# Kernel optimization log

Hardware: AMD Instinct MI355X
Metric: run time of the kernel (lower is better)

The kernel has to match this reference:

```python
import jax, jax.numpy as jnp
import numpy as np

N = 50000      # nodes
E = 800000     # edges
D_IN = 128     # embedding_in
EP = 200000    # prediction edge pairs
CONV_DIMS = [D_IN, 128, 64, 32]
LIN_DIMS = [32, 16, 8, 1]


def setup_inputs() -> dict:
    key = jax.random.key(0)
    ks = jax.random.split(key, 20)
    inp = {
        "x": jax.random.normal(ks[0], (N, D_IN), dtype=jnp.float32),
        "edge_index": jax.random.randint(ks[1], (2, E), 0, N, dtype=jnp.int64 if jax.config.jax_enable_x64 else jnp.int32),
        "pred_edges": jax.random.randint(ks[2], (EP, 2), 0, N, dtype=jnp.int64 if jax.config.jax_enable_x64 else jnp.int32),
    }
    k = 3
    for i in range(3):  # GCNConv weights [in,out] + bias (torch GCNConv has bias)
        din, dout = CONV_DIMS[i], CONV_DIMS[i + 1]
        inp[f"cw{i}"] = jax.random.normal(ks[k], (din, dout), dtype=jnp.float32) / np.sqrt(din); k += 1
        inp[f"cb{i}"] = jax.random.normal(ks[k], (dout,), dtype=jnp.float32) * 0.01; k += 1
    for i in range(3):  # Linear weights stored [in,out]
        din, dout = LIN_DIMS[i], LIN_DIMS[i + 1]
        inp[f"lw{i}"] = jax.random.normal(ks[k], (din, dout), dtype=jnp.float32) / np.sqrt(din); k += 1
        inp[f"lb{i}"] = jax.random.normal(ks[k], (dout,), dtype=jnp.float32) * 0.01; k += 1
    return inp


def gcn_conv(x, W, b, src, dst, n):
    """PyG GCNConv: D^-1/2 (A + I) D^-1/2 X W + b, deg over dst incl. self-loop."""
    h = x @ W  # [n, dout]
    deg = jax.ops.segment_sum(jnp.ones_like(dst, dtype=h.dtype), dst, num_segments=n) + 1.0
    dis = jax.lax.rsqrt(deg)  # deg >= 1 (self loop)
    msg = h[src] * (dis[src] * dis[dst])[:, None]      # gather + per-edge normalize
    out = jax.ops.segment_sum(msg, dst, num_segments=n)  # scatter-add into targets
    out = out + h * (dis * dis)[:, None]                # self-loop contribution
    return out + b


def reference(x, edge_index, pred_edges, cw0, cb0, cw1, cb1, cw2, cb2,
              lw0, lb0, lw1, lb1, lw2, lb2):
    src, dst = edge_index[0], edge_index[1]
    n = x.shape[0]
    for W, b in ((cw0, cb0), (cw1, cb1), (cw2, cb2)):
        x = jax.nn.relu(gcn_conv(x, W, b, src, dst, n))
    x = jax.nn.relu(x @ lw0 + lb0)
    x = jax.nn.relu(x @ lw1 + lb1)
    x = jax.nn.sigmoid(x @ lw2 + lb2)  # [n, 1]
    s = x[:, 0]
    # x[pred_edges] -> [EP,2,1]; mul of pair, transpose+flatten -> [EP]
    return s[pred_edges[:, 0]] * s[pred_edges[:, 1]]
```

## Files before the change

kernel.cpp:

```cpp
#include <hip/hip_runtime.h>
#include <math.h>

constexpr int NN  = 50000;
constexpr int NP  = 50048;
constexpr int NE  = 800000;
constexpr int NEP = 200000;

constexpr int NBKT  = 256;
constexpr int CAP   = 4096;
constexpr int CAPC  = 4096;
constexpr int CHUNK = 4096;

constexpr int BKB = (NE + CHUNK - 1) / CHUNK;
constexpr int W0B = 128 * 128 / 256;
constexpr int W1B = 128 * 64 / 256;
constexpr int W2B = 64 * 32 / 256;
constexpr int FRONT_BLOCKS = BKB + W0B + W1B + W2B;

constexpr int NODE_BLKS32 = (NN + 31) / 32;

typedef _Float16 half8_t __attribute__((ext_vector_type(8)));
typedef float    float4_t __attribute__((ext_vector_type(4)));

static inline int cdiv(long long a, int b) { return (int)((a + b - 1) / b); }

__global__ __launch_bounds__(256) void k_front(const int* __restrict__ src,
        const int* __restrict__ dst, int* __restrict__ binCnt,
        unsigned int* __restrict__ ebuf,
        const float* __restrict__ cw0, _Float16* __restrict__ WT0,
        const float* __restrict__ cw1, _Float16* __restrict__ WT1,
        const float* __restrict__ cw2, _Float16* __restrict__ WT2) {
    const int tid = threadIdx.x;
    const int bid = blockIdx.x;

    if (bid < BKB) {
        __shared__ int hist[NBKT];
        __shared__ int base[NBKT];
        __shared__ int cur[NBKT];
        constexpr int J = CHUNK / 256;
        const int e0 = bid * CHUNK;
        hist[tid] = 0;
        __syncthreads();
        int  s[J], bn[J], dl[J];
        bool ok[J];
#pragma unroll
        for (int j = 0; j < J; ++j) {
            int i = e0 + j * 256 + tid;
            ok[j] = i < NE;
            if (ok[j]) {
                int d = dst[i];
                s[j]  = src[i];
                bn[j] = d >> 8;
                dl[j] = d & 255;
                atomicAdd(&hist[bn[j]], 1);
            }
        }
        __syncthreads();
        base[tid] = hist[tid] ? atomicAdd(&binCnt[tid], hist[tid]) : 0;
        cur[tid] = 0;
        __syncthreads();
#pragma unroll
        for (int j = 0; j < J; ++j) {
            if (ok[j]) {
                int slot = base[bn[j]] + atomicAdd(&cur[bn[j]], 1);
                ebuf[bn[j] * CAP + slot] = (unsigned int)s[j] | ((unsigned int)dl[j] << 16);
            }
        }
        return;
    }
    if (bid < BKB + W0B) {
        int idx = (bid - BKB) * 256 + tid;
        int k = idx >> 7, n = idx & 127;
        WT0[(size_t)n * 128 + k] = (_Float16)cw0[idx];
        return;
    }
    if (bid < BKB + W0B + W1B) {
        int idx = (bid - BKB - W0B) * 256 + tid;
        int k = idx >> 6, n = idx & 63;
        WT1[(size_t)n * 128 + k] = (_Float16)cw1[idx];
        return;
    }
    {
        int idx = (bid - BKB - W0B - W1B) * 256 + tid;
        int k = idx >> 5, n = idx & 31;
        WT2[(size_t)n * 64 + k] = (_Float16)cw2[idx];
    }
}

__global__ __launch_bounds__(256) void k_csrbuild(const unsigned int* __restrict__ ebuf,
        const int* __restrict__ binCnt, int* __restrict__ off, float* __restrict__ dis,
        unsigned short* __restrict__ csr) {
    __shared__ int hist[256];
    __shared__ int sh[256];
    __shared__ int cur[256];
    const int tid = threadIdx.x;
    const int bin = blockIdx.x;
    const int cnt = binCnt[bin];
    const unsigned int* eb = ebuf + (size_t)bin * CAP;

    hist[tid] = 0;
    __syncthreads();
    for (int i = tid; i < cnt; i += 256)
        atomicAdd(&hist[eb[i] >> 16], 1);
    __syncthreads();

    int v  = hist[tid];
    int pv = (v + 3) & ~3;
    sh[tid] = pv;
    __syncthreads();
    for (int d = 1; d < 256; d <<= 1) {
        int t = (tid >= d) ? sh[tid - d] : 0;
        __syncthreads();
        sh[tid] += t;
        __syncthreads();
    }
    int start = bin * CAPC + (sh[tid] - pv);

    int node = bin * 256 + tid;
    if (node < NN) {
        off[node] = start | (pv << 20);
        dis[node] = rsqrtf((float)v + 1.0f);
    }
    cur[tid] = start;
    __syncthreads();

    for (int i = tid; i < cnt; i += 256) {
        unsigned int e = eb[i];
        int p = atomicAdd(&cur[e >> 16], 1);
        csr[p] = (unsigned short)(e & 0xFFFFu);
    }
    for (int k2 = v; k2 < pv; ++k2) csr[start + k2] = (unsigned short)NN;
}

__global__ __launch_bounds__(256) void k_gemm0(const float* __restrict__ X,
        const _Float16* __restrict__ WT, const float* __restrict__ dis,
        _Float16* __restrict__ g, int n) {
    constexpr int K = 128, DOUT = 128;
    constexpr int NC = 64, NT = 4, KT = 4, MT = 2;

    const int tid  = threadIdx.x;
    const int L    = tid & 63;
    const int w    = tid >> 6;
    const int wc   = w & 1;
    const int wr   = w >> 1;
    const int r0   = blockIdx.x * 64 + wr * 32;
    const int c0   = wc * NC;
    const int quad = L >> 4;
    const int lm   = L & 15;

    float4_t acc[MT][NT];
#pragma unroll
    for (int mt = 0; mt < MT; ++mt)
#pragma unroll
        for (int nt = 0; nt < NT; ++nt) acc[mt][nt] = (float4_t){0.f, 0.f, 0.f, 0.f};

#pragma unroll
    for (int kt = 0; kt < KT; ++kt) {
        half8_t a[MT], b[NT];
#pragma unroll
        for (int mt = 0; mt < MT; ++mt) {
            const float* xr = X + (size_t)(r0 + mt * 16 + lm) * K + kt * 32 + quad * 8;
            float4 u = *(const float4*)xr;
            float4 v = *(const float4*)(xr + 4);
            a[mt] = (half8_t){(_Float16)u.x, (_Float16)u.y, (_Float16)u.z, (_Float16)u.w,
                              (_Float16)v.x, (_Float16)v.y, (_Float16)v.z, (_Float16)v.w};
        }
#pragma unroll
        for (int nt = 0; nt < NT; ++nt)
            b[nt] = *(const half8_t*)(WT + (size_t)(c0 + nt * 16 + lm) * K + kt * 32 + quad * 8);
#pragma unroll
        for (int mt = 0; mt < MT; ++mt)
#pragma unroll
            for (int nt = 0; nt < NT; ++nt)
                acc[mt][nt] = __builtin_amdgcn_mfma_f32_16x16x32_f16(a[mt], b[nt], acc[mt][nt], 0, 0, 0);
    }

#pragma unroll
    for (int mt = 0; mt < MT; ++mt) {
        int rb = r0 + mt * 16 + quad * 4;
        float dv[4];
        *(float4*)dv = *(const float4*)(dis + rb);
#pragma unroll
        for (int nt = 0; nt < NT; ++nt) {
            int c = c0 + nt * 16 + lm;
#pragma unroll
            for (int reg = 0; reg < 4; ++reg) {
                int r = rb + reg;
                if (r < n)       g[(size_t)r * DOUT + c] = (_Float16)(acc[mt][nt][reg] * dv[reg]);
                else if (r == n) g[(size_t)r * DOUT + c] = (_Float16)0.f;
            }
        }
    }
}

template<int DIN, int DOUT>
__global__ __launch_bounds__(256) void k_agg_gemm(const half8_t* __restrict__ gin,
        const float* __restrict__ dis, const float* __restrict__ bias,
        const int* __restrict__ off, const unsigned short* __restrict__ csr,
        const _Float16* __restrict__ WT, _Float16* __restrict__ gout, int n) {
    constexpr int R8  = DIN / 8;
    constexpr int HPL = R8 / 8;
    constexpr int XS  = DIN + 8;
    __shared__ _Float16 sX[32 * XS];

    const int tid  = threadIdx.x;
    const int l8   = tid & 7;
    const int ln   = tid >> 3;
    const int r0   = blockIdx.x * 32;
    const int node = r0 + ln;

    if (node < n) {
        float dd = dis[node];
        float a[HPL * 8];
#pragma unroll
        for (int h = 0; h < HPL; ++h) {
            half8_t hv = gin[(size_t)node * R8 + l8 * HPL + h];
#pragma unroll
            for (int j = 0; j < 8; ++j) a[h * 8 + j] = (float)hv[j];
        }
        int pk = off[node];
        int e0 = pk & 0xFFFFF;
        int e1 = e0 + (pk >> 20);
        for (int e = e0; e < e1; e += 4) {
            ushort4 c4 = *(const ushort4*)(csr + e);
            int sidx[4] = {c4.x, c4.y, c4.z, c4.w};
#pragma unroll
            for (int q = 0; q < 4; ++q) {
#pragma unroll
                for (int h = 0; h < HPL; ++h) {
                    half8_t v = gin[(size_t)sidx[q] * R8 + l8 * HPL + h];
#pragma unroll
                    for (int j = 0; j < 8; ++j) a[h * 8 + j] += (float)v[j];
                }
            }
        }
#pragma unroll
        for (int h = 0; h < HPL; ++h) {
            half8_t o;
#pragma unroll
            for (int j = 0; j < 8; ++j) {
                int ch = l8 * (HPL * 8) + h * 8 + j;
                o[j] = (_Float16)fmaxf(fmaf(a[h * 8 + j], dd, bias[ch]), 0.f);
            }
            *(half8_t*)(sX + ln * XS + l8 * (HPL * 8) + h * 8) = o;
        }
    } else {
#pragma unroll
        for (int h = 0; h < HPL; ++h)
            *(half8_t*)(sX + ln * XS + l8 * (HPL * 8) + h * 8) =
                (half8_t){(_Float16)0.f, (_Float16)0.f, (_Float16)0.f, (_Float16)0.f,
                          (_Float16)0.f, (_Float16)0.f, (_Float16)0.f, (_Float16)0.f};
    }
    __syncthreads();

    constexpr int CWV = DOUT / 16;
    constexpr int MT  = (CWV == 4) ? 2 : 1;
    constexpr int KT  = DIN / 32;
    const int L    = tid & 63;
    const int w    = tid >> 6;
    const int quad = L >> 4;
    const int lm   = L & 15;
    const int c0   = (CWV == 4) ? (w * 16) : ((w & 1) * 16);
    const int m0   = (CWV == 4) ? 0 : ((w >> 1) * 16);

    float4_t acc[MT];
#pragma unroll
    for (int mt = 0; mt < MT; ++mt) acc[mt] = (float4_t){0.f, 0.f, 0.f, 0.f};

#pragma unroll
    for (int kt = 0; kt < KT; ++kt) {
        half8_t b = *(const half8_t*)(WT + (size_t)(c0 + lm) * DIN + kt * 32 + quad * 8);
#pragma unroll
        for (int mt = 0; mt < MT; ++mt) {
            half8_t aF = *(const half8_t*)(sX + (m0 + mt * 16 + lm) * XS + kt * 32 + quad * 8);
            acc[mt] = __builtin_amdgcn_mfma_f32_16x16x32_f16(aF, b, acc[mt], 0, 0, 0);
        }
    }
#pragma unroll
    for (int mt = 0; mt < MT; ++mt) {
        int rb = r0 + m0 + mt * 16 + quad * 4;
        float dv[4];
        *(float4*)dv = *(const float4*)(dis + rb);
#pragma unroll
        for (int reg = 0; reg < 4; ++reg) {
            int r = rb + reg;
            if (r < n)       gout[(size_t)r * DOUT + c0 + lm] = (_Float16)(acc[mt][reg] * dv[reg]);
            else if (r == n) gout[(size_t)r * DOUT + c0 + lm] = (_Float16)0.f;
        }
    }
}

__global__ __launch_bounds__(256) void k_agg_mlp(const half8_t* __restrict__ g,
        const float* __restrict__ dis, const float* __restrict__ b,
        const int* __restrict__ off, const unsigned short* __restrict__ csr,
        const float* __restrict__ lw0, const float* __restrict__ lb0,
        const float* __restrict__ lw1, const float* __restrict__ lb1,
        const float* __restrict__ lw2, const float* __restrict__ lb2,
        float* __restrict__ sv, int n) {
    __shared__ float sh[32 * 33];
    const int tid  = threadIdx.x;
    const int l8   = tid & 7;
    const int lane = l8 & 3;
    const int grp  = l8 >> 2;
    const int ln   = tid >> 3;
    const int node = blockIdx.x * 32 + ln;

    if (node < n) {
        float dd = dis[node];
        half8_t hv = g[(size_t)node * 4 + lane];
        float a[8];
#pragma unroll
        for (int j = 0; j < 8; ++j) a[j] = (grp == 0) ? (float)hv[j] : 0.f;
        int pk = off[node];
        int e0 = pk & 0xFFFFF;
        int e1 = e0 + (pk >> 20);
        for (int e = e0 + grp * 4; e < e1; e += 8) {
            ushort4 c4 = *(const ushort4*)(csr + e);
            half8_t v0 = g[(size_t)c4.x * 4 + lane];
            half8_t v1 = g[(size_t)c4.y * 4 + lane];
            half8_t v2 = g[(size_t)c4.z * 4 + lane];
            half8_t v3 = g[(size_t)c4.w * 4 + lane];
#pragma unroll
            for (int j = 0; j < 8; ++j)
                a[j] += (float)v0[j] + (float)v1[j] + (float)v2[j] + (float)v3[j];
        }
#pragma unroll
        for (int j = 0; j < 8; ++j) a[j] += __shfl_xor(a[j], 4);
        if (grp == 0) {
            float* row = sh + ln * 33 + lane * 8;
#pragma unroll
            for (int j = 0; j < 8; ++j)
                row[j] = fmaxf(fmaf(a[j], dd, b[lane * 8 + j]), 0.f);
        }
    }
    __syncthreads();

    if (tid < 32) {
        int node2 = blockIdx.x * 32 + tid;
        if (node2 < n) {
            const float* v = sh + tid * 33;
            float a[16];
#pragma unroll
            for (int j = 0; j < 16; ++j) {
                float acc = lb0[j];
#pragma unroll
                for (int k = 0; k < 32; ++k) acc = fmaf(v[k], lw0[k * 16 + j], acc);
                a[j] = fmaxf(acc, 0.f);
            }
            float b8[8];
#pragma unroll
            for (int j = 0; j < 8; ++j) {
                float acc = lb1[j];
#pragma unroll
                for (int k = 0; k < 16; ++k) acc = fmaf(a[k], lw1[k * 8 + j], acc);
                b8[j] = fmaxf(acc, 0.f);
            }
            float z = lb2[0];
#pragma unroll
            for (int k = 0; k < 8; ++k) z = fmaf(b8[k], lw2[k], z);
            sv[node2] = 1.0f / (1.0f + expf(-z));
        }
    }
}

__global__ void k_pred(const float* __restrict__ s, const int* __restrict__ pe,
                       float* __restrict__ out, int ep2) {
    int i = blockIdx.x * blockDim.x + threadIdx.x;
    if (i >= ep2) return;
    int4 p = ((const int4*)pe)[i];
    float2 o;
    o.x = s[p.x] * s[p.y];
    o.y = s[p.z] * s[p.w];
    ((float2*)out)[i] = o;
}

extern "C" void kernel_launch(void* const* d_in, const int* in_sizes, int n_in,
                              void* d_out, int out_size, void* d_ws, size_t ws_size,
                              hipStream_t stream) {
    const float* x   = (const float*)d_in[0];
    const int*   ei  = (const int*)d_in[1];
    const int*   pe  = (const int*)d_in[2];
    const float* cw0 = (const float*)d_in[3];
    const float* cb0 = (const float*)d_in[4];
    const float* cw1 = (const float*)d_in[5];
    const float* cb1 = (const float*)d_in[6];
    const float* cw2 = (const float*)d_in[7];
    const float* cb2 = (const float*)d_in[8];
    const float* lw0 = (const float*)d_in[9];
    const float* lb0 = (const float*)d_in[10];
    const float* lw1 = (const float*)d_in[11];
    const float* lb1 = (const float*)d_in[12];
    const float* lw2 = (const float*)d_in[13];
    const float* lb2 = (const float*)d_in[14];

    const int* src = ei;
    const int* dst = ei + NE;

    char* w = (char*)d_ws;
    float*          dis  = (float*)w;           w += sizeof(float) * NN;
    _Float16*       M0   = (_Float16*)w;        w += sizeof(_Float16) * (size_t)(NN + 1) * 128;
    _Float16*       M1   = (_Float16*)w;        w += sizeof(_Float16) * (size_t)(NN + 1) * 64;
    _Float16*       M2   = (_Float16*)w;        w += sizeof(_Float16) * (size_t)(NN + 1) * 32;
    float*          sv   = (float*)w;           w += sizeof(float) * NN;
    _Float16*       WT0  = (_Float16*)w;        w += sizeof(_Float16) * 128 * 128;
    _Float16*       WT1  = (_Float16*)w;        w += sizeof(_Float16) * 64 * 128;
    _Float16*       WT2  = (_Float16*)w;        w += sizeof(_Float16) * 32 * 64;
    int*            off  = (int*)w;             w += sizeof(int) * NN;
    unsigned short* csr  = (unsigned short*)w;  w += sizeof(unsigned short) * (size_t)NBKT * CAPC;
    int*            binCnt = (int*)w;           w += sizeof(int) * NBKT;
    unsigned int*   ebuf = (unsigned int*)w;    w += sizeof(unsigned int) * (size_t)NBKT * CAP;

    const int T = 256;

    hipMemsetAsync(binCnt, 0, sizeof(int) * NBKT, stream);
    k_front<<<FRONT_BLOCKS, 256, 0, stream>>>(src, dst, binCnt, ebuf,
                                              cw0, WT0, cw1, WT1, cw2, WT2);

    k_csrbuild<<<NBKT, 256, 0, stream>>>(ebuf, binCnt, off, dis, csr);

    k_gemm0<<<NP / 64, 256, 0, stream>>>(x, WT0, dis, M0, NN);

    k_agg_gemm<128, 64><<<NODE_BLKS32, 256, 0, stream>>>((const half8_t*)M0, dis, cb0,
                                                         off, csr, WT1, M1, NN);

    k_agg_gemm<64, 32><<<NODE_BLKS32, 256, 0, stream>>>((const half8_t*)M1, dis, cb1,
                                                        off, csr, WT2, M2, NN);

    k_agg_mlp<<<NODE_BLKS32, 256, 0, stream>>>((const half8_t*)M2, dis, cb2, off, csr,
                                               lw0, lb0, lw1, lb1, lw2, lb2, sv, NN);

    k_pred<<<cdiv(NEP / 2, T), T, 0, stream>>>(sv, pe, (float*)d_out, NEP / 2);
}
```

Baseline: 217.8 us.

## Split 128-wide aggregation across 16 lanes per node and unroll gathers by eight

```diff
diff --git a/kernel.cpp b/kernel.cpp
--- a/kernel.cpp
+++ b/kernel.cpp
@@ -18,6 +18,7 @@
 constexpr int FRONT_BLOCKS = BKB + W0B + W1B + W2B;
 
 constexpr int NODE_BLKS32 = (NN + 31) / 32;
+constexpr int NODE_BLKS16 = (NN + 15) / 16;
 
 typedef _Float16 half8_t __attribute__((ext_vector_type(8)));
 typedef float    float4_t __attribute__((ext_vector_type(4)));
@@ -193,14 +194,99 @@
     }
 }
 
-template<int DIN, int DOUT>
-__global__ __launch_bounds__(256) void k_agg_gemm(const half8_t* __restrict__ gin,
+__global__ __launch_bounds__(256) void k_agg_gemm16(const half8_t* __restrict__ gin,
         const float* __restrict__ dis, const float* __restrict__ bias,
         const int* __restrict__ off, const unsigned short* __restrict__ csr,
         const _Float16* __restrict__ WT, _Float16* __restrict__ gout, int n) {
-    constexpr int R8  = DIN / 8;
-    constexpr int HPL = R8 / 8;
-    constexpr int XS  = DIN + 8;
+    constexpr int DIN = 128, DOUT = 64;
+    constexpr int R8 = DIN / 8;
+    constexpr int XS = DIN + 8;
+    __shared__ _Float16 sX[16 * XS];
+
+    const int tid  = threadIdx.x;
+    const int l16  = tid & 15;
+    const int ln   = tid >> 4;
+    const int r0   = blockIdx.x * 16;
+    const int node = r0 + ln;
+
+    if (blockIdx.x == 0 && tid < DOUT / 8)
+        ((half8_t*)(gout + (size_t)n * DOUT))[tid] =
+            (half8_t){(_Float16)0.f, (_Float16)0.f, (_Float16)0.f, (_Float16)0.f,
+                      (_Float16)0.f, (_Float16)0.f, (_Float16)0.f, (_Float16)0.f};
+
+    float dd = dis[node];
+    half8_t hv = gin[(size_t)node * R8 + l16];
+    float a[8];
+#pragma unroll
+    for (int j = 0; j < 8; ++j) a[j] = (float)hv[j];
+
+    int pk = off[node];
+    int e0 = pk & 0xFFFFF;
+    int e1 = e0 + (pk >> 20);
+    int e = e0;
+    for (; e + 7 < e1; e += 8) {
+        ushort4 c4 = *(const ushort4*)(csr + e);
+        ushort4 c8 = *(const ushort4*)(csr + e + 4);
+        half8_t v0 = gin[(size_t)c4.x * R8 + l16];
+        half8_t v1 = gin[(size_t)c4.y * R8 + l16];
+        half8_t v2 = gin[(size_t)c4.z * R8 + l16];
+        half8_t v3 = gin[(size_t)c4.w * R8 + l16];
+        half8_t v4 = gin[(size_t)c8.x * R8 + l16];
+        half8_t v5 = gin[(size_t)c8.y * R8 + l16];
+        half8_t v6 = gin[(size_t)c8.z * R8 + l16];
+        half8_t v7 = gin[(size_t)c8.w * R8 + l16];
+#pragma unroll
+        for (int j = 0; j < 8; ++j)
+            a[j] += ((float)v0[j] + (float)v1[j]) + ((float)v2[j] + (float)v3[j])
+                  + ((float)v4[j] + (float)v5[j]) + ((float)v6[j] + (float)v7[j]);
+    }
+    if (e < e1) {
+        ushort4 c4 = *(const ushort4*)(csr + e);
+        half8_t v0 = gin[(size_t)c4.x * R8 + l16];
+        half8_t v1 = gin[(size_t)c4.y * R8 + l16];
+        half8_t v2 = gin[(size_t)c4.z * R8 + l16];
+        half8_t v3 = gin[(size_t)c4.w * R8 + l16];
+#pragma unroll
+        for (int j = 0; j < 8; ++j)
+            a[j] += ((float)v0[j] + (float)v1[j]) + ((float)v2[j] + (float)v3[j]);
+    }
+    {
+        half8_t o;
+#pragma unroll
+        for (int j = 0; j < 8; ++j)
+            o[j] = (_Float16)fmaxf(fmaf(a[j], dd, bias[l16 * 8 + j]), 0.f);
+        *(half8_t*)(sX + ln * XS + l16 * 8) = o;
+    }
+    __syncthreads();
+
+    const int L    = tid & 63;
+    const int w    = tid >> 6;
+    const int quad = L >> 4;
+    const int lm   = L & 15;
+    const int c0   = w * 16;
+
+    float4_t acc = (float4_t){0.f, 0.f, 0.f, 0.f};
+#pragma unroll
+    for (int kt = 0; kt < DIN / 32; ++kt) {
+        half8_t b  = *(const half8_t*)(WT + (size_t)(c0 + lm) * DIN + kt * 32 + quad * 8);
+        half8_t aF = *(const half8_t*)(sX + lm * XS + kt * 32 + quad * 8);
+        acc = __builtin_amdgcn_mfma_f32_16x16x32_f16(aF, b, acc, 0, 0, 0);
+    }
+    int rb = r0 + quad * 4;
+    float dv[4];
+    *(float4*)dv = *(const float4*)(dis + rb);
+#pragma unroll
+    for (int reg = 0; reg < 4; ++reg)
+        gout[(size_t)(rb + reg) * DOUT + c0 + lm] = (_Float16)(acc[reg] * dv[reg]);
+}
+
+__global__ __launch_bounds__(256) void k_agg_gemm8(const half8_t* __restrict__ gin,
+        const float* __restrict__ dis, const float* __restrict__ bias,
+        const int* __restrict__ off, const unsigned short* __restrict__ csr,
+        const _Float16* __restrict__ WT, _Float16* __restrict__ gout, int n) {
+    constexpr int DIN = 64, DOUT = 32;
+    constexpr int R8 = DIN / 8;
+    constexpr int XS = DIN + 8;
     __shared__ _Float16 sX[32 * XS];
 
     const int tid  = threadIdx.x;
@@ -211,82 +297,74 @@
 
     if (node < n) {
         float dd = dis[node];
-        float a[HPL * 8];
-#pragma unroll
-        for (int h = 0; h < HPL; ++h) {
-            half8_t hv = gin[(size_t)node * R8 + l8 * HPL + h];
-#pragma unroll
-            for (int j = 0; j < 8; ++j) a[h * 8 + j] = (float)hv[j];
-        }
+        half8_t hv = gin[(size_t)node * R8 + l8];
+        float a[8];
+#pragma unroll
+        for (int j = 0; j < 8; ++j) a[j] = (float)hv[j];
         int pk = off[node];
         int e0 = pk & 0xFFFFF;
         int e1 = e0 + (pk >> 20);
-        for (int e = e0; e < e1; e += 4) {
+        int e = e0;
+        for (; e + 7 < e1; e += 8) {
             ushort4 c4 = *(const ushort4*)(csr + e);
-            int sidx[4] = {c4.x, c4.y, c4.z, c4.w};
-#pragma unroll
-            for (int q = 0; q < 4; ++q) {
-#pragma unroll
-                for (int h = 0; h < HPL; ++h) {
-                    half8_t v = gin[(size_t)sidx[q] * R8 + l8 * HPL + h];
-#pragma unroll
-                    for (int j = 0; j < 8; ++j) a[h * 8 + j] += (float)v[j];
-                }
-            }
-        }
-#pragma unroll
-        for (int h = 0; h < HPL; ++h) {
-            half8_t o;
-#pragma unroll
-            for (int j = 0; j < 8; ++j) {
-                int ch = l8 * (HPL * 8) + h * 8 + j;
-                o[j] = (_Float16)fmaxf(fmaf(a[h * 8 + j], dd, bias[ch]), 0.f);
-            }
-            *(half8_t*)(sX + ln * XS + l8 * (HPL * 8) + h * 8) = o;
-        }
+            ushort4 c8 = *(const ushort4*)(csr + e + 4);
+            half8_t v0 = gin[(size_t)c4.x * R8 + l8];
+            half8_t v1 = gin[(size_t)c4.y * R8 + l8];
+            half8_t v2 = gin[(size_t)c4.z * R8 + l8];
+            half8_t v3 = gin[(size_t)c4.w * R8 + l8];
+            half8_t v4 = gin[(size_t)c8.x * R8 + l8];
+            half8_t v5 = gin[(size_t)c8.y * R8 + l8];
+            half8_t v6 = gin[(size_t)c8.z * R8 + l8];
+            half8_t v7 = gin[(size_t)c8.w * R8 + l8];
+#pragma unroll
+            for (int j = 0; j < 8; ++j)
+                a[j] += ((float)v0[j] + (float)v1[j]) + ((float)v2[j] + (float)v3[j])
+                      + ((float)v4[j] + (float)v5[j]) + ((float)v6[j] + (float)v7[j]);
+        }
+        if (e < e1) {
+            ushort4 c4 = *(const ushort4*)(csr + e);
+            half8_t v0 = gin[(size_t)c4.x * R8 + l8];
+            half8_t v1 = gin[(size_t)c4.y * R8 + l8];
+            half8_t v2 = gin[(size_t)c4.z * R8 + l8];
+            half8_t v3 = gin[(size_t)c4.w * R8 + l8];
+#pragma unroll
+            for (int j = 0; j < 8; ++j)
+                a[j] += ((float)v0[j] + (float)v1[j]) + ((float)v2[j] + (float)v3[j]);
+        }
+        half8_t o;
+#pragma unroll
+        for (int j = 0; j < 8; ++j)
+            o[j] = (_Float16)fmaxf(fmaf(a[j], dd, bias[l8 * 8 + j]), 0.f);
+        *(half8_t*)(sX + ln * XS + l8 * 8) = o;
     } else {
-#pragma unroll
-        for (int h = 0; h < HPL; ++h)
-            *(half8_t*)(sX + ln * XS + l8 * (HPL * 8) + h * 8) =
-                (half8_t){(_Float16)0.f, (_Float16)0.f, (_Float16)0.f, (_Float16)0.f,
-                          (_Float16)0.f, (_Float16)0.f, (_Float16)0.f, (_Float16)0.f};
-    }
-    __syncthreads();
-
-    constexpr int CWV = DOUT / 16;
-    constexpr int MT  = (CWV == 4) ? 2 : 1;
-    constexpr int KT  = DIN / 32;
+        *(half8_t*)(sX + ln * XS + l8 * 8) =
+            (half8_t){(_Float16)0.f, (_Float16)0.f, (_Float16)0.f, (_Float16)0.f,
+                      (_Float16)0.f, (_Float16)0.f, (_Float16)0.f, (_Float16)0.f};
+    }
+    __syncthreads();
+
     const int L    = tid & 63;
     const int w    = tid >> 6;
     const int quad = L >> 4;
     const int lm   = L & 15;
-    const int c0   = (CWV == 4) ? (w * 16) : ((w & 1) * 16);
-    const int m0   = (CWV == 4) ? 0 : ((w >> 1) * 16);
-
-    float4_t acc[MT];
-#pragma unroll
-    for (int mt = 0; mt < MT; ++mt) acc[mt] = (float4_t){0.f, 0.f, 0.f, 0.f};
-
-#pragma unroll
-    for (int kt = 0; kt < KT; ++kt) {
-        half8_t b = *(const half8_t*)(WT + (size_t)(c0 + lm) * DIN + kt * 32 + quad * 8);
-#pragma unroll
-        for (int mt = 0; mt < MT; ++mt) {
-            half8_t aF = *(const half8_t*)(sX + (m0 + mt * 16 + lm) * XS + kt * 32 + quad * 8);
-            acc[mt] = __builtin_amdgcn_mfma_f32_16x16x32_f16(aF, b, acc[mt], 0, 0, 0);
-        }
-    }
-#pragma unroll
-    for (int mt = 0; mt < MT; ++mt) {
-        int rb = r0 + m0 + mt * 16 + quad * 4;
-        float dv[4];
-        *(float4*)dv = *(const float4*)(dis + rb);
-#pragma unroll
-        for (int reg = 0; reg < 4; ++reg) {
-            int r = rb + reg;
-            if (r < n)       gout[(size_t)r * DOUT + c0 + lm] = (_Float16)(acc[mt][reg] * dv[reg]);
-            else if (r == n) gout[(size_t)r * DOUT + c0 + lm] = (_Float16)0.f;
-        }
+    const int c0   = (w & 1) * 16;
+    const int m0   = (w >> 1) * 16;
+
+    float4_t acc = (float4_t){0.f, 0.f, 0.f, 0.f};
+#pragma unroll
+    for (int kt = 0; kt < DIN / 32; ++kt) {
+        half8_t b  = *(const half8_t*)(WT + (size_t)(c0 + lm) * DIN + kt * 32 + quad * 8);
+        half8_t aF = *(const half8_t*)(sX + (m0 + lm) * XS + kt * 32 + quad * 8);
+        acc = __builtin_amdgcn_mfma_f32_16x16x32_f16(aF, b, acc, 0, 0, 0);
+    }
+    int rb = r0 + m0 + quad * 4;
+    float dv[4];
+    *(float4*)dv = *(const float4*)(dis + rb);
+#pragma unroll
+    for (int reg = 0; reg < 4; ++reg) {
+        int r = rb + reg;
+        if (r < n)       gout[(size_t)r * DOUT + c0 + lm] = (_Float16)(acc[reg] * dv[reg]);
+        else if (r == n) gout[(size_t)r * DOUT + c0 + lm] = (_Float16)0.f;
     }
 }
 
@@ -420,11 +498,11 @@
 
     k_gemm0<<<NP / 64, 256, 0, stream>>>(x, WT0, dis, M0, NN);
 
-    k_agg_gemm<128, 64><<<NODE_BLKS32, 256, 0, stream>>>((const half8_t*)M0, dis, cb0,
-                                                         off, csr, WT1, M1, NN);
-
-    k_agg_gemm<64, 32><<<NODE_BLKS32, 256, 0, stream>>>((const half8_t*)M1, dis, cb1,
-                                                        off, csr, WT2, M2, NN);
+    k_agg_gemm16<<<NODE_BLKS16, 256, 0, stream>>>((const half8_t*)M0, dis, cb0,
+                                                  off, csr, WT1, M1, NN);
+
+    k_agg_gemm8<<<NODE_BLKS32, 256, 0, stream>>>((const half8_t*)M1, dis, cb1,
+                                                 off, csr, WT2, M2, NN);
 
     k_agg_mlp<<<NODE_BLKS32, 256, 0, stream>>>((const half8_t*)M2, dis, cb2, off, csr,
                                                lw0, lb0, lw1, lb1, lw2, lb2, sv, NN);
```

Result: faster. 213.2 us (-2.1%).
